# Performance work log

Measured on AMD Instinct MI355X. Metric: run time of the kernel, lower is better.

The kernel has to match this reference:

```python
import jax, jax.numpy as jnp
import numpy as np

CUTOFF = 5.0  # Angstrom contact cutoff for atom interaction mask
N, L, ATOMS, D, H = 1, 64, 14, 128, 64
M = L * ATOMS  # 896 atoms


def atom_interaction_mask_batch(pos14, ppi_code, cutoff=CUTOFF):
    # pos14: (N, L, 14, 3), ppi_code: (N, L) -> mask (N, L*14, L*14)
    n, l = ppi_code.shape
    pos = pos14.reshape(n, l * ATOMS, 3)
    d2 = jnp.sum((pos[:, :, None, :] - pos[:, None, :, :]) ** 2, axis=-1)  # (N,M,M)
    codes = jnp.repeat(ppi_code, ATOMS, axis=1)  # (N,M)
    cross_chain = codes[:, :, None] != codes[:, None, :]
    return (d2 < cutoff * cutoff) & cross_chain


def _edge_feats(feats, W1, b1, mask):
    # Decompose fc_1(concat(f_i, f_j)) = f_i @ W1[:, :D].T + f_j @ W1[:, D:].T + b1
    # so the (N,M,M,2D) concat tensor is never materialized.
    d = feats.shape[-1]
    hi = feats @ W1[:, :d].T  # (N,M,H)
    hj = feats @ W1[:, d:].T  # (N,M,H)
    e = hi[:, :, None, :] + hj[:, None, :, :] + b1  # (N,M,M,H)
    return jnp.where(mask[..., None], e, 0.0)


def setup_inputs() -> dict:
    key = jax.random.key(0)
    ks = jax.random.split(key, 8)
    feats_wt = jax.random.normal(ks[0], (N, M, D), dtype=jnp.float32)
    feats_mut = jax.random.normal(ks[1], (N, M, D), dtype=jnp.float32)
    # scale positions so the 5A cutoff yields a sparse, realistic contact mask
    pos14_wt = jax.random.normal(ks[2], (N, L, ATOMS, 3), dtype=jnp.float32) * 10.0
    pos14_mut = pos14_wt + jax.random.normal(ks[3], (N, L, ATOMS, 3), dtype=jnp.float32) * 0.5
    ppi_code_wt = jax.random.randint(ks[4], (N, L), 0, 2)
    ppi_code_mut = ppi_code_wt
    # fc_1: Linear(2D -> H), fc_2: Linear(H -> 1), torch layout W:(out,in)
    W1 = jax.random.normal(ks[5], (H, 2 * D), dtype=jnp.float32) / np.sqrt(2 * D)
    b1 = jnp.zeros((H,), dtype=jnp.float32)
    W2 = jax.random.normal(ks[6], (1, H), dtype=jnp.float32) / np.sqrt(H)
    b2 = jnp.zeros((1,), dtype=jnp.float32)
    return dict(feats_wt=feats_wt, feats_mut=feats_mut, pos14_wt=pos14_wt,
                pos14_mut=pos14_mut, ppi_code_wt=ppi_code_wt,
                ppi_code_mut=ppi_code_mut, W1=W1, b1=b1, W2=W2, b2=b2)


def reference(feats_wt, feats_mut, pos14_wt, pos14_mut, ppi_code_wt,
              ppi_code_mut, W1, b1, W2, b2):
    mask_wt = atom_interaction_mask_batch(pos14_wt, ppi_code_wt)
    mask_mut = atom_interaction_mask_batch(pos14_mut, ppi_code_mut)
    e_wt = _edge_feats(feats_wt, W1, b1, mask_wt)    # (N,M,M,H)
    e_mut = _edge_feats(feats_mut, W1, b1, mask_mut)  # (N,M,M,H)
    diff = e_mut - e_wt
    n = diff.shape[0]
    # (n, l1, 14, l2, 14, H) -> sum over residues l1, l2 -> (n, 14, 14, H)
    blocks = diff.reshape(n, L, ATOMS, L, ATOMS, H).sum(axis=(1, 3))
    out = blocks @ W2.T + b2  # (n,14,14,1)
    return out.reshape(n, -1)  # (n, 196)
```

## Files before the change

### kernel.cpp

```cpp
#include <hip/hip_runtime.h>

#define LRES   64
#define ATOMS  14
#define M      896
#define DF     128
#define HF     64
#define CUT2   25.0f

__global__ __launch_bounds__(256) void k_fused(
    const float* __restrict__ feats_wt, const float* __restrict__ feats_mut,
    const float* __restrict__ pos_wt,   const float* __restrict__ pos_mut,
    const int* __restrict__ ppi_wt,     const int* __restrict__ ppi_mut,
    const float* __restrict__ W1, const float* __restrict__ b1,
    const float* __restrict__ W2, const float* __restrict__ b2,
    float* __restrict__ out)
{
    const int b  = blockIdx.x;
    const int a1 = b / ATOMS, a2 = b % ATOMS;
    const int t  = threadIdx.x;

    __shared__ float u[DF], v[DF];
    __shared__ float pA[2][3][LRES];
    __shared__ float pB[2][3][LRES];
    __shared__ int   pp[2][LRES];
    __shared__ float part[LRES];
    __shared__ float sbs;

    {
        const int grp = t >> 6;
        const int l   = t & 63;
        const int st  = grp >> 1;
        const int sl  = (grp & 1) ? a2 : a1;
        const float* ps = st ? pos_mut : pos_wt;
        const float* p  = ps + (l * ATOMS + sl) * 3;
        const float x = p[0], y = p[1], z = p[2];
        if (grp & 1) { pB[st][0][l] = x; pB[st][1][l] = y; pB[st][2][l] = z; }
        else         { pA[st][0][l] = x; pA[st][1][l] = y; pA[st][2][l] = z; }
        if (grp == 0) pp[0][l] = ppi_wt[l];
        if (grp == 1) pp[1][l] = ppi_mut[l];
    }

    {
        const int d = t & 127;
        const float* col = W1 + d + ((t >> 7) ? DF : 0);
        float s = 0.f;
        #pragma unroll
        for (int h = 0; h < HF; ++h) s += W2[h] * col[h * (2 * DF)];
        if (t < 128) u[d] = s; else v[d] = s;
    }

    if (t < 64) {
        float sbp = W2[t] * b1[t];
        #pragma unroll
        for (int off = 32; off > 0; off >>= 1) sbp += __shfl_down(sbp, off);
        if (t == 0) sbs = sbp;
    }

    __syncthreads();

    const int l1 = t >> 2;
    const int c  = t & 3;
    const int i_row = l1 * ATOMS + a1;
    const int j_col = l1 * ATOMS + a2;

    const int myw = pp[0][l1], mym = pp[1][l1];
    const float rwx = pA[0][0][l1], rwy = pA[0][1][l1], rwz = pA[0][2][l1];
    const float rmx = pA[1][0][l1], rmy = pA[1][1][l1], rmz = pA[1][2][l1];
    const float cwx = pB[0][0][l1], cwy = pB[0][1][l1], cwz = pB[0][2][l1];
    const float cmx = pB[1][0][l1], cmy = pB[1][1][l1], cmz = pB[1][2][l1];

    int cw_r = 0, cm_r = 0, cw_c = 0, cm_c = 0;
    #pragma unroll
    for (int k = 0; k < 16; ++k) {
        const int l2 = (k << 2) | c;
        if (pp[0][l2] != myw) {
            float dx = rwx - pB[0][0][l2], dy = rwy - pB[0][1][l2], dz = rwz - pB[0][2][l2];
            if (dx*dx + dy*dy + dz*dz < CUT2) ++cw_r;
            dx = cwx - pA[0][0][l2]; dy = cwy - pA[0][1][l2]; dz = cwz - pA[0][2][l2];
            if (dx*dx + dy*dy + dz*dz < CUT2) ++cw_c;
        }
        if (pp[1][l2] != mym) {
            float dx = rmx - pB[1][0][l2], dy = rmy - pB[1][1][l2], dz = rmz - pB[1][2][l2];
            if (dx*dx + dy*dy + dz*dz < CUT2) ++cm_r;
            dx = cmx - pA[1][0][l2]; dy = cmy - pA[1][1][l2]; dz = cmz - pA[1][2][l2];
            if (dx*dx + dy*dy + dz*dz < CUT2) ++cm_c;
        }
    }

    float si_w = 0.f, si_m = 0.f, sj_w = 0.f, sj_m = 0.f;
    {
        const float4* fw_r = (const float4*)(feats_wt  + i_row * DF);
        const float4* fm_r = (const float4*)(feats_mut + i_row * DF);
        const float4* fw_c = (const float4*)(feats_wt  + j_col * DF);
        const float4* fm_c = (const float4*)(feats_mut + j_col * DF);
        const float4* u4 = (const float4*)u;
        const float4* v4 = (const float4*)v;
        #pragma unroll
        for (int q = c * 8; q < c * 8 + 8; ++q) {
            const float4 uu = u4[q], vv = v4[q];
            float4 a = fw_r[q];
            si_w += a.x*uu.x + a.y*uu.y + a.z*uu.z + a.w*uu.w;
            a = fm_r[q];
            si_m += a.x*uu.x + a.y*uu.y + a.z*uu.z + a.w*uu.w;
            a = fw_c[q];
            sj_w += a.x*vv.x + a.y*vv.y + a.z*vv.z + a.w*vv.w;
            a = fm_c[q];
            sj_m += a.x*vv.x + a.y*vv.y + a.z*vv.z + a.w*vv.w;
        }
    }

    #pragma unroll
    for (int off = 2; off > 0; off >>= 1) {
        si_w += __shfl_down(si_w, off, 4);
        si_m += __shfl_down(si_m, off, 4);
        sj_w += __shfl_down(sj_w, off, 4);
        sj_m += __shfl_down(sj_m, off, 4);
        cw_r += __shfl_down(cw_r, off, 4);
        cm_r += __shfl_down(cm_r, off, 4);
        cw_c += __shfl_down(cw_c, off, 4);
        cm_c += __shfl_down(cm_c, off, 4);
    }
    if (c == 0) {
        const float sb = sbs;
        part[l1] = (si_m + sb) * (float)cm_r - (si_w + sb) * (float)cw_r
                 +  sj_m * (float)cm_c       -  sj_w * (float)cw_c;
    }
    __syncthreads();

    if (t < 64) {
        float s = part[t];
        #pragma unroll
        for (int off = 32; off > 0; off >>= 1) s += __shfl_down(s, off);
        if (t == 0) out[b] = s + b2[0];
    }
}

extern "C" void kernel_launch(void* const* d_in, const int* in_sizes, int n_in,
                              void* d_out, int out_size, void* d_ws, size_t ws_size,
                              hipStream_t stream) {
    const float* feats_wt  = (const float*)d_in[0];
    const float* feats_mut = (const float*)d_in[1];
    const float* pos_wt    = (const float*)d_in[2];
    const float* pos_mut   = (const float*)d_in[3];
    const int*   ppi_wt    = (const int*)d_in[4];
    const int*   ppi_mut   = (const int*)d_in[5];
    const float* W1        = (const float*)d_in[6];
    const float* b1        = (const float*)d_in[7];
    const float* W2        = (const float*)d_in[8];
    const float* b2        = (const float*)d_in[9];
    float* out = (float*)d_out;

    k_fused<<<ATOMS * ATOMS, 256, 0, stream>>>(
        feats_wt, feats_mut, pos_wt, pos_mut, ppi_wt, ppi_mut,
        W1, b1, W2, b2, out);
}
```

Before: 18.15 us.

## Prefetch feature rows into registers and overlap W1 loads with contact counting

Issues all global loads of the four feature-row slices into registers at kernel start and batches the 64 W1 column loads into a register array before the contact-count loop, so memory latency overlaps with the distance computation instead of being serialized. Positions are stored as float4 in shared memory for single-load access, and the u/v vectors are stored in a padded float4 layout indexed per lane group. This adds an extra barrier and raises register pressure (32 float4 plus 64 floats per thread), which can reduce occupancy.

```diff
diff --git a/kernel.cpp b/kernel.cpp
--- a/kernel.cpp
+++ b/kernel.cpp
@@ -2,7 +2,6 @@
 
 #define LRES   64
 #define ATOMS  14
-#define M      896
 #define DF     128
 #define HF     64
 #define CUT2   25.0f
@@ -18,13 +17,30 @@
     const int b  = blockIdx.x;
     const int a1 = b / ATOMS, a2 = b % ATOMS;
     const int t  = threadIdx.x;
+    const int l1 = t >> 2;
+    const int c  = t & 3;
+    const int i_row = l1 * ATOMS + a1;
+    const int j_col = l1 * ATOMS + a2;
 
-    __shared__ float u[DF], v[DF];
-    __shared__ float pA[2][3][LRES];
-    __shared__ float pB[2][3][LRES];
-    __shared__ int   pp[2][LRES];
-    __shared__ float part[LRES];
-    __shared__ float sbs;
+    __shared__ float4 posA[2][LRES];
+    __shared__ float4 posB[2][LRES];
+    __shared__ int    pp[2][LRES];
+    __shared__ float4 uv4[2][4][9];
+    __shared__ float  part[LRES];
+    __shared__ float  sbs;
+
+    float4 frw[8], frm[8], fcw[8], fcm[8];
+    {
+        const float4* pfrw = (const float4*)(feats_wt  + i_row * DF) + c * 8;
+        const float4* pfrm = (const float4*)(feats_mut + i_row * DF) + c * 8;
+        const float4* pfcw = (const float4*)(feats_wt  + j_col * DF) + c * 8;
+        const float4* pfcm = (const float4*)(feats_mut + j_col * DF) + c * 8;
+        #pragma unroll
+        for (int q = 0; q < 8; ++q) {
+            frw[q] = pfrw[q]; frm[q] = pfrm[q];
+            fcw[q] = pfcw[q]; fcm[q] = pfcm[q];
+        }
+    }
 
     {
         const int grp = t >> 6;
@@ -33,20 +49,10 @@
         const int sl  = (grp & 1) ? a2 : a1;
         const float* ps = st ? pos_mut : pos_wt;
         const float* p  = ps + (l * ATOMS + sl) * 3;
-        const float x = p[0], y = p[1], z = p[2];
-        if (grp & 1) { pB[st][0][l] = x; pB[st][1][l] = y; pB[st][2][l] = z; }
-        else         { pA[st][0][l] = x; pA[st][1][l] = y; pA[st][2][l] = z; }
+        float4 q; q.x = p[0]; q.y = p[1]; q.z = p[2]; q.w = 0.f;
+        if (grp & 1) posB[st][l] = q; else posA[st][l] = q;
         if (grp == 0) pp[0][l] = ppi_wt[l];
         if (grp == 1) pp[1][l] = ppi_mut[l];
-    }
-
-    {
-        const int d = t & 127;
-        const float* col = W1 + d + ((t >> 7) ? DF : 0);
-        float s = 0.f;
-        #pragma unroll
-        for (int h = 0; h < HF; ++h) s += W2[h] * col[h * (2 * DF)];
-        if (t < 128) u[d] = s; else v[d] = s;
     }
 
     if (t < 64) {
@@ -58,55 +64,60 @@
 
     __syncthreads();
 
-    const int l1 = t >> 2;
-    const int c  = t & 3;
-    const int i_row = l1 * ATOMS + a1;
-    const int j_col = l1 * ATOMS + a2;
+    const int d = t & 127;
+    const float* col = W1 + d + ((t >> 7) ? DF : 0);
+    float w1v[HF];
+    #pragma unroll
+    for (int h = 0; h < HF; ++h) w1v[h] = col[h * (2 * DF)];
 
+    const float4 rw = posA[0][l1], rm = posA[1][l1];
+    const float4 cw = posB[0][l1], cmv = posB[1][l1];
     const int myw = pp[0][l1], mym = pp[1][l1];
-    const float rwx = pA[0][0][l1], rwy = pA[0][1][l1], rwz = pA[0][2][l1];
-    const float rmx = pA[1][0][l1], rmy = pA[1][1][l1], rmz = pA[1][2][l1];
-    const float cwx = pB[0][0][l1], cwy = pB[0][1][l1], cwz = pB[0][2][l1];
-    const float cmx = pB[1][0][l1], cmy = pB[1][1][l1], cmz = pB[1][2][l1];
-
     int cw_r = 0, cm_r = 0, cw_c = 0, cm_c = 0;
     #pragma unroll
     for (int k = 0; k < 16; ++k) {
         const int l2 = (k << 2) | c;
-        if (pp[0][l2] != myw) {
-            float dx = rwx - pB[0][0][l2], dy = rwy - pB[0][1][l2], dz = rwz - pB[0][2][l2];
+        const int pw = pp[0][l2], pm = pp[1][l2];
+        const float4 bw = posB[0][l2], aw = posA[0][l2];
+        const float4 bm = posB[1][l2], am = posA[1][l2];
+        if (pw != myw) {
+            float dx = rw.x - bw.x, dy = rw.y - bw.y, dz = rw.z - bw.z;
             if (dx*dx + dy*dy + dz*dz < CUT2) ++cw_r;
-            dx = cwx - pA[0][0][l2]; dy = cwy - pA[0][1][l2]; dz = cwz - pA[0][2][l2];
+            dx = cw.x - aw.x; dy = cw.y - aw.y; dz = cw.z - aw.z;
             if (dx*dx + dy*dy + dz*dz < CUT2) ++cw_c;
         }
-        if (pp[1][l2] != mym) {
-            float dx = rmx - pB[1][0][l2], dy = rmy - pB[1][1][l2], dz = rmz - pB[1][2][l2];
+        if (pm != mym) {
+            float dx = rm.x - bm.x, dy = rm.y - bm.y, dz = rm.z - bm.z;
             if (dx*dx + dy*dy + dz*dz < CUT2) ++cm_r;
-            dx = cmx - pA[1][0][l2]; dy = cmy - pA[1][1][l2]; dz = cmz - pA[1][2][l2];
+            dx = cmv.x - am.x; dy = cmv.y - am.y; dz = cmv.z - am.z;
             if (dx*dx + dy*dy + dz*dz < CUT2) ++cm_c;
         }
     }
 
+    {
+        float s0 = 0.f, s1 = 0.f, s2 = 0.f, s3 = 0.f;
+        #pragma unroll
+        for (int h = 0; h < HF; h += 4) {
+            s0 += W2[h]     * w1v[h];
+            s1 += W2[h + 1] * w1v[h + 1];
+            s2 += W2[h + 2] * w1v[h + 2];
+            s3 += W2[h + 3] * w1v[h + 3];
+        }
+        const float s = (s0 + s1) + (s2 + s3);
+        float* up = (float*)&uv4[t >> 7][d >> 5][(d >> 2) & 7];
+        up[d & 3] = s;
+    }
+    __syncthreads();
+
     float si_w = 0.f, si_m = 0.f, sj_w = 0.f, sj_m = 0.f;
-    {
-        const float4* fw_r = (const float4*)(feats_wt  + i_row * DF);
-        const float4* fm_r = (const float4*)(feats_mut + i_row * DF);
-        const float4* fw_c = (const float4*)(feats_wt  + j_col * DF);
-        const float4* fm_c = (const float4*)(feats_mut + j_col * DF);
-        const float4* u4 = (const float4*)u;
-        const float4* v4 = (const float4*)v;
-        #pragma unroll
-        for (int q = c * 8; q < c * 8 + 8; ++q) {
-            const float4 uu = u4[q], vv = v4[q];
-            float4 a = fw_r[q];
-            si_w += a.x*uu.x + a.y*uu.y + a.z*uu.z + a.w*uu.w;
-            a = fm_r[q];
-            si_m += a.x*uu.x + a.y*uu.y + a.z*uu.z + a.w*uu.w;
-            a = fw_c[q];
-            sj_w += a.x*vv.x + a.y*vv.y + a.z*vv.z + a.w*vv.w;
-            a = fm_c[q];
-            sj_m += a.x*vv.x + a.y*vv.y + a.z*vv.z + a.w*vv.w;
-        }
+    #pragma unroll
+    for (int q = 0; q < 8; ++q) {
+        const float4 uu = uv4[0][c][q];
+        const float4 vv = uv4[1][c][q];
+        si_w += frw[q].x*uu.x + frw[q].y*uu.y + frw[q].z*uu.z + frw[q].w*uu.w;
+        si_m += frm[q].x*uu.x + frm[q].y*uu.y + frm[q].z*uu.z + frm[q].w*uu.w;
+        sj_w += fcw[q].x*vv.x + fcw[q].y*vv.y + fcw[q].z*vv.z + fcw[q].w*vv.w;
+        sj_m += fcm[q].x*vv.x + fcm[q].y*vv.y + fcm[q].z*vv.z + fcm[q].w*vv.w;
     }
 
     #pragma unroll
```

Result: faster. 16.28 us (-10.3%).
